# Kernel optimization log

Measured on AMD Instinct MI355X. Metric: run time of the kernel, lower is better.

## Reference

```python
import jax, jax.numpy as jnp
import numpy as np

D = 768
H = 12
HD = 64
S = 77
FF = 3072
EPS = 1e-5


def _layernorm(x, w, b):
    mu = jnp.mean(x, axis=-1, keepdims=True)
    var = jnp.mean(jnp.square(x - mu), axis=-1, keepdims=True)
    return (x - mu) * jax.lax.rsqrt(var + EPS) * w + b


def setup_inputs() -> dict:
    key = jax.random.key(0)
    ks = jax.random.split(key, 18)
    s = 1.0 / np.sqrt(D)
    sf = 1.0 / np.sqrt(FF)
    return {
        "x": jax.random.normal(ks[0], (512, S, D), dtype=jnp.float32),
        "ln1_w": jnp.ones((D,), jnp.float32),
        "ln1_b": jnp.zeros((D,), jnp.float32),
        "qw": jax.random.uniform(ks[1], (D, D), jnp.float32, -s, s),
        "qb": jax.random.uniform(ks[2], (D,), jnp.float32, -s, s),
        "kw": jax.random.uniform(ks[3], (D, D), jnp.float32, -s, s),
        "kb": jax.random.uniform(ks[4], (D,), jnp.float32, -s, s),
        "vw": jax.random.uniform(ks[5], (D, D), jnp.float32, -s, s),
        "vb": jax.random.uniform(ks[6], (D,), jnp.float32, -s, s),
        "ow": jax.random.uniform(ks[7], (D, D), jnp.float32, -s, s),
        "ob": jax.random.uniform(ks[8], (D,), jnp.float32, -s, s),
        "ln2_w": jnp.ones((D,), jnp.float32),
        "ln2_b": jnp.zeros((D,), jnp.float32),
        "fc1_w": jax.random.uniform(ks[9], (FF, D), jnp.float32, -s, s),
        "fc1_b": jax.random.uniform(ks[10], (FF,), jnp.float32, -s, s),
        "fc2_w": jax.random.uniform(ks[11], (D, FF), jnp.float32, -sf, sf),
        "fc2_b": jax.random.uniform(ks[12], (D,), jnp.float32, -sf, sf),
    }


def reference(x, ln1_w, ln1_b, qw, qb, kw, kb, vw, vb, ow, ob,
              ln2_w, ln2_b, fc1_w, fc1_b, fc2_w, fc2_b):
    B = x.shape[0]
    # --- attention block ---
    h = _layernorm(x, ln1_w, ln1_b)
    q = (h @ qw.T + qb) * 0.125
    k = h @ kw.T + kb
    v = h @ vw.T + vb
    # [B, S, H, HD] -> [B, H, S, HD]
    q = q.reshape(B, S, H, HD).transpose(0, 2, 1, 3)
    k = k.reshape(B, S, H, HD).transpose(0, 2, 1, 3)
    v = v.reshape(B, S, H, HD).transpose(0, 2, 1, 3)
    scores = jnp.einsum('bhqd,bhkd->bhqk', q, k)  # [B,H,S,S]
    # causal additive mask: -inf strictly above diagonal
    mask = jnp.triu(jnp.full((S, S), -jnp.inf, dtype=scores.dtype), 1)
    scores = scores + mask
    attn = jax.nn.softmax(scores, axis=-1)
    ctx = jnp.einsum('bhqk,bhkd->bhqd', attn, v)  # [B,H,S,HD]
    ctx = ctx.transpose(0, 2, 1, 3).reshape(B, S, D)
    x = x + (ctx @ ow.T + ob)
    # --- MLP block with QuickGELU ---
    res = x
    h2 = _layernorm(x, ln2_w, ln2_b) @ fc1_w.T + fc1_b
    h2 = h2 * jax.nn.sigmoid(h2 * 1.702)
    return res + (h2 @ fc2_w.T + fc2_b)
```

## Files before the change

### kernel.cpp

```cpp
#include <hip/hip_runtime.h>

typedef unsigned short u16;
typedef __bf16 v8bf __attribute__((ext_vector_type(8)));
typedef unsigned short u16x8 __attribute__((ext_vector_type(8)));
typedef float v4f __attribute__((ext_vector_type(4)));

#define DEV __device__ __forceinline__

constexpr int M_TOK = 512 * 77;

DEV u16 f2bf(float f) {
  union { float f; unsigned int u; } v; v.f = f;
  unsigned int r = v.u + 0x7fffu + ((v.u >> 16) & 1u);
  return (u16)(r >> 16);
}

DEV void gload16(const void* g, void* l) {
  __builtin_amdgcn_global_load_lds((const __attribute__((address_space(1))) void*)g,
                                   (__attribute__((address_space(3))) void*)l, 16, 0, 0);
}

DEV v4f MF(v8bf a, v8bf b, v4f c) {
  return __builtin_amdgcn_mfma_f32_16x16x32_bf16(a, b, c, 0, 0, 0);
}

__global__ void cvt4_k(const float* __restrict__ src, u16* __restrict__ dst, int n4, float scale) {
  int i = blockIdx.x * blockDim.x + threadIdx.x;
  if (i >= n4) return;
  const float4 v = ((const float4*)src)[i];
  ushort4 o;
  o.x = f2bf(v.x * scale); o.y = f2bf(v.y * scale);
  o.z = f2bf(v.z * scale); o.w = f2bf(v.w * scale);
  ((ushort4*)dst)[i] = o;
}

__global__ void qkvb_k(const float* __restrict__ qb, const float* __restrict__ kb,
                       const float* __restrict__ vb, float* __restrict__ dst) {
  int i = blockIdx.x * 256 + threadIdx.x;
  if (i >= 2304) return;
  dst[i] = (i < 768) ? qb[i] * 0.125f : (i < 1536 ? kb[i - 768] : vb[i - 1536]);
}

__global__ __launch_bounds__(256) void ln_k(const float* __restrict__ x, const float* __restrict__ w,
                                            const float* __restrict__ bvec, u16* __restrict__ out, int nrows) {
  const int lane = threadIdx.x & 63;
  const int row = blockIdx.x * 4 + (threadIdx.x >> 6);
  if (row >= nrows) return;
  const float4* xr = (const float4*)(x + (size_t)row * 768);
  float4 v[3];
  float sum = 0.f, sq = 0.f;
#pragma unroll
  for (int t = 0; t < 3; ++t) {
    v[t] = xr[lane + 64 * t];
    sum += v[t].x + v[t].y + v[t].z + v[t].w;
    sq  += v[t].x * v[t].x + v[t].y * v[t].y + v[t].z * v[t].z + v[t].w * v[t].w;
  }
#pragma unroll
  for (int o = 1; o < 64; o <<= 1) { sum += __shfl_xor(sum, o, 64); sq += __shfl_xor(sq, o, 64); }
  const float mean = sum * (1.f / 768.f);
  const float inv = rsqrtf(sq * (1.f / 768.f) - mean * mean + 1e-5f);
  u16* orow = out + (size_t)row * 768;
#pragma unroll
  for (int t = 0; t < 3; ++t) {
    const int c = 4 * (lane + 64 * t);
    ushort4 o4;
    o4.x = f2bf((v[t].x - mean) * inv * w[c + 0] + bvec[c + 0]);
    o4.y = f2bf((v[t].y - mean) * inv * w[c + 1] + bvec[c + 1]);
    o4.z = f2bf((v[t].z - mean) * inv * w[c + 2] + bvec[c + 2]);
    o4.w = f2bf((v[t].w - mean) * inv * w[c + 3] + bvec[c + 3]);
    *(ushort4*)(orow + c) = o4;
  }
}

template <int OUTF32, int ACT, int RES>
__global__ __launch_bounds__(512, 2) void gemm256_k(
    const u16* __restrict__ A, const u16* __restrict__ Bw,
    const float* __restrict__ bias, const float* __restrict__ res,
    void* __restrict__ out, int M, int N, int K, int nbx) {
  __shared__ u16 lds[65536];
  const int tid = threadIdx.x;
  const int lane = tid & 63;
  const int wv = tid >> 6;
  const int wr = wv >> 2, wc = wv & 3;

  const int nwg = gridDim.x;
  const int q = nwg >> 3, r8 = nwg & 7;
  const int xcd = blockIdx.x & 7, cidx = blockIdx.x >> 3;
  const int wg = (xcd < r8 ? xcd * (q + 1) : r8 * (q + 1) + (xcd - r8) * q) + cidx;
  const int m0 = (wg / nbx) * 256;
  const int n0 = (wg % nbx) * 256;

  const int frow = lane & 15;
  const int fq = lane >> 4;
  const int chunkp = (fq ^ (lane & 3) ^ ((lane >> 2) & 3)) & 3;
  const int aRd = (wr * 128 + frow) * 32 + chunkp * 8;
  const int bRd = (wc * 64 + frow) * 32 + chunkp * 8;

  const int srow = tid >> 2;
  const int scg = ((tid & 3) ^ (srow & 3) ^ ((srow >> 2) & 3)) & 3;
  const size_t aBase = (size_t)(m0 + srow) * K + scg * 8;
  const size_t bBase = (size_t)(n0 + srow) * K + scg * 8;
  const int ldsW = wv * 512;

#define GLDA(kt, g) gload16(A + aBase + (size_t)(g) * 128 * K + (kt) * 32, \
                            &lds[(((kt) & 3) << 14) + ((g) << 12) + ldsW])
#define GLDB(kt, g) gload16(Bw + bBase + (size_t)(g) * 128 * K + (kt) * 32, \
                            &lds[(((kt) & 3) << 14) + 8192 + ((g) << 12) + ldsW])
#define BAR() asm volatile("s_barrier" ::: "memory")

  v4f acc[8][4];
#pragma unroll
  for (int i = 0; i < 8; ++i)
#pragma unroll
    for (int j = 0; j < 4; ++j) acc[i][j] = (v4f){0.f, 0.f, 0.f, 0.f};

  const int NT = K >> 5;

  GLDA(0, 0); GLDA(0, 1); GLDB(0, 0); GLDB(0, 1);
  GLDA(1, 0); GLDA(1, 1); GLDB(1, 0); GLDB(1, 1);
  GLDA(2, 0); GLDA(2, 1); GLDB(2, 0); GLDB(2, 1);
  asm volatile("s_waitcnt vmcnt(8)" ::: "memory");
  BAR();

#define KTILE(kt, STG, VM)                                                      \
  do {                                                                          \
    const int sb = ((kt) & 3) << 14;                                            \
    v8bf fa0 = *(const v8bf*)&lds[sb + aRd +    0];                             \
    v8bf fa1 = *(const v8bf*)&lds[sb + aRd +  512];                             \
    v8bf fa2 = *(const v8bf*)&lds[sb + aRd + 1024];                             \
    v8bf fa3 = *(const v8bf*)&lds[sb + aRd + 1536];                             \
    v8bf fb0 = *(const v8bf*)&lds[sb + 8192 + bRd +    0];                      \
    v8bf fb1 = *(const v8bf*)&lds[sb + 8192 + bRd +  512];                      \
    v8bf fb2 = *(const v8bf*)&lds[sb + 8192 + bRd + 1024];                      \
    v8bf fb3 = *(const v8bf*)&lds[sb + 8192 + bRd + 1536];                      \
    if (STG) { GLDA((kt) + 3, 0); GLDA((kt) + 3, 1); }                          \
    BAR();                                                                      \
    __builtin_amdgcn_s_setprio(1);                                              \
    acc[0][0] = MF(fa0, fb0, acc[0][0]); acc[0][1] = MF(fa0, fb1, acc[0][1]);   \
    acc[0][2] = MF(fa0, fb2, acc[0][2]); acc[0][3] = MF(fa0, fb3, acc[0][3]);   \
    acc[1][0] = MF(fa1, fb0, acc[1][0]); acc[1][1] = MF(fa1, fb1, acc[1][1]);   \
    acc[1][2] = MF(fa1, fb2, acc[1][2]); acc[1][3] = MF(fa1, fb3, acc[1][3]);   \
    acc[2][0] = MF(fa2, fb0, acc[2][0]); acc[2][1] = MF(fa2, fb1, acc[2][1]);   \
    acc[2][2] = MF(fa2, fb2, acc[2][2]); acc[2][3] = MF(fa2, fb3, acc[2][3]);   \
    acc[3][0] = MF(fa3, fb0, acc[3][0]); acc[3][1] = MF(fa3, fb1, acc[3][1]);   \
    acc[3][2] = MF(fa3, fb2, acc[3][2]); acc[3][3] = MF(fa3, fb3, acc[3][3]);   \
    __builtin_amdgcn_s_setprio(0);                                              \
    BAR();                                                                      \
    v8bf fa4 = *(const v8bf*)&lds[sb + aRd + 2048];                             \
    v8bf fa5 = *(const v8bf*)&lds[sb + aRd + 2560];                             \
    v8bf fa6 = *(const v8bf*)&lds[sb + aRd + 3072];                             \
    v8bf fa7 = *(const v8bf*)&lds[sb + aRd + 3584];                             \
    if (STG) { GLDB((kt) + 3, 0); GLDB((kt) + 3, 1); }                          \
    if ((VM) == 8) asm volatile("s_waitcnt vmcnt(8)" ::: "memory");             \
    else if ((VM) == 4) asm volatile("s_waitcnt vmcnt(4)" ::: "memory");        \
    else if ((VM) == 0) asm volatile("s_waitcnt vmcnt(0)" ::: "memory");        \
    BAR();                                                                      \
    __builtin_amdgcn_s_setprio(1);                                              \
    acc[4][0] = MF(fa4, fb0, acc[4][0]); acc[4][1] = MF(fa4, fb1, acc[4][1]);   \
    acc[4][2] = MF(fa4, fb2, acc[4][2]); acc[4][3] = MF(fa4, fb3, acc[4][3]);   \
    acc[5][0] = MF(fa5, fb0, acc[5][0]); acc[5][1] = MF(fa5, fb1, acc[5][1]);   \
    acc[5][2] = MF(fa5, fb2, acc[5][2]); acc[5][3] = MF(fa5, fb3, acc[5][3]);   \
    acc[6][0] = MF(fa6, fb0, acc[6][0]); acc[6][1] = MF(fa6, fb1, acc[6][1]);   \
    acc[6][2] = MF(fa6, fb2, acc[6][2]); acc[6][3] = MF(fa6, fb3, acc[6][3]);   \
    acc[7][0] = MF(fa7, fb0, acc[7][0]); acc[7][1] = MF(fa7, fb1, acc[7][1]);   \
    acc[7][2] = MF(fa7, fb2, acc[7][2]); acc[7][3] = MF(fa7, fb3, acc[7][3]);   \
    __builtin_amdgcn_s_setprio(0);                                              \
    BAR();                                                                      \
  } while (0)

  for (int kt = 0; kt + 3 < NT; ++kt) KTILE(kt, 1, 8);
  KTILE(NT - 3, 0, 4);
  KTILE(NT - 2, 0, 0);
  KTILE(NT - 1, 0, -1);
#undef KTILE
#undef GLDA
#undef GLDB
#undef BAR

#pragma unroll
  for (int i = 0; i < 8; ++i) {
    const int rowb = m0 + wr * 128 + i * 16 + fq * 4;
#pragma unroll
    for (int j = 0; j < 4; ++j) {
      const int col = n0 + wc * 64 + j * 16 + frow;
      const float bv = bias[col];
#pragma unroll
      for (int rr = 0; rr < 4; ++rr) {
        float v = acc[i][j][rr] + bv;
        if (ACT) v = v * (1.f / (1.f + __expf(-1.702f * v)));
        const size_t off = (size_t)(rowb + rr) * N + col;
        if (RES) v += res[off];
        if (OUTF32) ((float*)out)[off] = v;
        else ((u16*)out)[off] = f2bf(v);
      }
    }
  }
}

__global__ __launch_bounds__(256) void attn_k(const u16* __restrict__ qkv, u16* __restrict__ ctx) {
  __shared__ u16 sQK[10240];
  __shared__ u16 sVt[64 * 120];
  __shared__ float sS[80][81];
  const int tid = threadIdx.x;
  const int lane = tid & 63;
  const int wv = tid >> 6;
  const int b = blockIdx.x / 12;
  const int h = blockIdx.x % 12;
  u16* sQ = sQK;
  u16* sK = sQK + 5120;
  u16* sP = sQK;

  for (int i = tid; i < 10240 + 64 * 120; i += 256) {
    if (i < 10240) sQK[i] = 0; else sVt[i - 10240] = 0;
  }
  __syncthreads();

  const size_t tokBase = (size_t)(b * 77) * 2304 + h * 64;
  for (int c = tid; c < 77 * 8; c += 256) {
    const int row = c >> 3, k8 = (c & 7) * 8;
    const size_t src = tokBase + (size_t)row * 2304 + k8;
    *(u16x8*)&sQ[row * 64 + k8] = *(const u16x8*)&qkv[src];
    *(u16x8*)&sK[row * 64 + k8] = *(const u16x8*)&qkv[src + 768];
    u16x8 v = *(const u16x8*)&qkv[src + 1536];
#pragma unroll
    for (int j = 0; j < 8; ++j) sVt[(k8 + j) * 120 + row] = v[j];
  }
  __syncthreads();

  const int frow = lane & 15, fk = (lane >> 4) * 8;
  for (int t = wv; t < 25; t += 4) {
    const int it = t / 5, jt = t % 5;
    v4f acc = {0.f, 0.f, 0.f, 0.f};
#pragma unroll
    for (int kk = 0; kk < 2; ++kk) {
      v8bf a = *(const v8bf*)&sQ[(it * 16 + frow) * 64 + kk * 32 + fk];
      v8bf bb = *(const v8bf*)&sK[(jt * 16 + frow) * 64 + kk * 32 + fk];
      acc = MF(a, bb, acc);
    }
    const int col = jt * 16 + frow;
#pragma unroll
    for (int r = 0; r < 4; ++r) {
      const int row = it * 16 + (lane >> 4) * 4 + r;
      sS[row][col] = (col > row) ? -1e30f : acc[r];
    }
  }
  __syncthreads();

  if (tid < 80) {
    const int row = tid;
    float mx = -1e30f;
    for (int c2 = 0; c2 < 80; ++c2) mx = fmaxf(mx, sS[row][c2]);
    float sum = 0.f;
    for (int c2 = 0; c2 < 80; ++c2) { float e = __expf(sS[row][c2] - mx); sum += e; sS[row][c2] = e; }
    const float inv = 1.f / sum;
    for (int c2 = 0; c2 < 80; ++c2) sP[row * 96 + c2] = f2bf(sS[row][c2] * inv);
    for (int c2 = 80; c2 < 96; ++c2) sP[row * 96 + c2] = 0;
  }
  __syncthreads();

  const size_t outBase = (size_t)(b * 77) * 768 + h * 64;
  for (int t = wv; t < 20; t += 4) {
    const int it = t / 4, jt = t % 4;
    v4f acc = {0.f, 0.f, 0.f, 0.f};
#pragma unroll
    for (int kk = 0; kk < 3; ++kk) {
      v8bf a = *(const v8bf*)&sP[(it * 16 + frow) * 96 + kk * 32 + fk];
      v8bf bb = *(const v8bf*)&sVt[(jt * 16 + frow) * 120 + kk * 32 + fk];
      acc = MF(a, bb, acc);
    }
    const int col = jt * 16 + frow;
#pragma unroll
    for (int r = 0; r < 4; ++r) {
      const int row = it * 16 + (lane >> 4) * 4 + r;
      if (row < 77) ctx[outBase + (size_t)row * 768 + col] = f2bf(acc[r]);
    }
  }
}

extern "C" void kernel_launch(void* const* d_in, const int* in_sizes, int n_in,
                              void* d_out, int out_size, void* d_ws, size_t ws_size,
                              hipStream_t stream) {
  const float* x    = (const float*)d_in[0];
  const float* ln1w = (const float*)d_in[1];
  const float* ln1b = (const float*)d_in[2];
  const float* qw   = (const float*)d_in[3];
  const float* qb   = (const float*)d_in[4];
  const float* kw   = (const float*)d_in[5];
  const float* kb   = (const float*)d_in[6];
  const float* vw   = (const float*)d_in[7];
  const float* vb   = (const float*)d_in[8];
  const float* ow   = (const float*)d_in[9];
  const float* ob   = (const float*)d_in[10];
  const float* ln2w = (const float*)d_in[11];
  const float* ln2b = (const float*)d_in[12];
  const float* f1wf = (const float*)d_in[13];
  const float* f1b  = (const float*)d_in[14];
  const float* f2wf = (const float*)d_in[15];
  const float* f2b  = (const float*)d_in[16];
  float* outp = (float*)d_out;

  char* p = (char*)d_ws;
  auto alloc = [&](size_t bytes) { char* r = p; p += (bytes + 255) & ~(size_t)255; return r; };
  u16* wqkv = (u16*)alloc((size_t)2304 * 768 * 2);
  u16* owb  = (u16*)alloc((size_t)768 * 768 * 2);
  u16* f1w  = (u16*)alloc((size_t)3072 * 768 * 2);
  u16* f2w  = (u16*)alloc((size_t)768 * 3072 * 2);
  float* qkvb = (float*)alloc(2304 * 4);
  u16* bufA = (u16*)alloc((size_t)M_TOK * 768 * 2);
  u16* bufB = (u16*)alloc((size_t)M_TOK * 3072 * 2);

  cvt4_k<<<576, 256, 0, stream>>>(qw, wqkv, 147456, 0.125f);
  cvt4_k<<<576, 256, 0, stream>>>(kw, wqkv + 589824, 147456, 1.f);
  cvt4_k<<<576, 256, 0, stream>>>(vw, wqkv + 1179648, 147456, 1.f);
  cvt4_k<<<576, 256, 0, stream>>>(ow, owb, 147456, 1.f);
  cvt4_k<<<2304, 256, 0, stream>>>(f1wf, f1w, 589824, 1.f);
  cvt4_k<<<2304, 256, 0, stream>>>(f2wf, f2w, 589824, 1.f);
  qkvb_k<<<9, 256, 0, stream>>>(qb, kb, vb, qkvb);

  ln_k<<<M_TOK / 4, 256, 0, stream>>>(x, ln1w, ln1b, bufA, M_TOK);
  gemm256_k<0, 0, 0><<<154 * 9, 512, 0, stream>>>(bufA, wqkv, qkvb, nullptr, bufB, M_TOK, 2304, 768, 9);
  attn_k<<<512 * 12, 256, 0, stream>>>(bufB, bufA);
  gemm256_k<1, 0, 1><<<154 * 3, 512, 0, stream>>>(bufA, owb, ob, x, outp, M_TOK, 768, 768, 3);
  ln_k<<<M_TOK / 4, 256, 0, stream>>>(outp, ln2w, ln2b, bufA, M_TOK);
  gemm256_k<0, 1, 0><<<154 * 12, 512, 0, stream>>>(bufA, f1w, f1b, nullptr, bufB, M_TOK, 3072, 768, 12);
  gemm256_k<1, 0, 1><<<154 * 3, 512, 0, stream>>>(bufB, f2w, f2b, outp, outp, M_TOK, 768, 3072, 3);
}
```

Baseline: 976.4 us.

## Shrink GEMM tile to 128x256 with double-buffered LDS and higher occupancy

Reduces the GEMM block tile from 256x256 to 128x256. The LDS pipeline drops from a 4-stage ring to 2-stage double buffering, and launch bounds rise to 4 blocks per CU. The aim is more concurrent blocks and better latency hiding through occupancy, with smaller LDS and register use per block. In exchange, arithmetic intensity per block is lower and prefetch depth is shorter, which may expose global load latency.

```diff
diff --git a/kernel.cpp b/kernel.cpp
--- a/kernel.cpp
+++ b/kernel.cpp
@@ -73,11 +73,11 @@
 }
 
 template <int OUTF32, int ACT, int RES>
-__global__ __launch_bounds__(512, 2) void gemm256_k(
+__global__ __launch_bounds__(512, 4) void gemm_k(
     const u16* __restrict__ A, const u16* __restrict__ Bw,
     const float* __restrict__ bias, const float* __restrict__ res,
     void* __restrict__ out, int M, int N, int K, int nbx) {
-  __shared__ u16 lds[65536];
+  __shared__ u16 lds[24576];
   const int tid = threadIdx.x;
   const int lane = tid & 63;
   const int wv = tid >> 6;
@@ -87,14 +87,14 @@
   const int q = nwg >> 3, r8 = nwg & 7;
   const int xcd = blockIdx.x & 7, cidx = blockIdx.x >> 3;
   const int wg = (xcd < r8 ? xcd * (q + 1) : r8 * (q + 1) + (xcd - r8) * q) + cidx;
-  const int m0 = (wg / nbx) * 256;
+  const int m0 = (wg / nbx) * 128;
   const int n0 = (wg % nbx) * 256;
 
   const int frow = lane & 15;
   const int fq = lane >> 4;
   const int chunkp = (fq ^ (lane & 3) ^ ((lane >> 2) & 3)) & 3;
-  const int aRd = (wr * 128 + frow) * 32 + chunkp * 8;
-  const int bRd = (wc * 64 + frow) * 32 + chunkp * 8;
+  const int aRd = (wr * 64 + frow) * 32 + chunkp * 8;
+  const int bRd = 4096 + (wc * 64 + frow) * 32 + chunkp * 8;
 
   const int srow = tid >> 2;
   const int scg = ((tid & 3) ^ (srow & 3) ^ ((srow >> 2) & 3)) & 3;
@@ -102,39 +102,41 @@
   const size_t bBase = (size_t)(n0 + srow) * K + scg * 8;
   const int ldsW = wv * 512;
 
-#define GLDA(kt, g) gload16(A + aBase + (size_t)(g) * 128 * K + (kt) * 32, \
-                            &lds[(((kt) & 3) << 14) + ((g) << 12) + ldsW])
-#define GLDB(kt, g) gload16(Bw + bBase + (size_t)(g) * 128 * K + (kt) * 32, \
-                            &lds[(((kt) & 3) << 14) + 8192 + ((g) << 12) + ldsW])
+#define GLDA(kt) gload16(A + aBase + (size_t)(kt) * 32, \
+                         &lds[(((kt) & 1) ? 12288 : 0) + ldsW])
+#define GLDB(kt, g) gload16(Bw + bBase + (size_t)(g) * 128 * K + (size_t)(kt) * 32, \
+                            &lds[(((kt) & 1) ? 12288 : 0) + 4096 + ((g) << 12) + ldsW])
 #define BAR() asm volatile("s_barrier" ::: "memory")
 
-  v4f acc[8][4];
-#pragma unroll
-  for (int i = 0; i < 8; ++i)
+  v4f acc[4][4];
+#pragma unroll
+  for (int i = 0; i < 4; ++i)
 #pragma unroll
     for (int j = 0; j < 4; ++j) acc[i][j] = (v4f){0.f, 0.f, 0.f, 0.f};
 
   const int NT = K >> 5;
 
-  GLDA(0, 0); GLDA(0, 1); GLDB(0, 0); GLDB(0, 1);
-  GLDA(1, 0); GLDA(1, 1); GLDB(1, 0); GLDB(1, 1);
-  GLDA(2, 0); GLDA(2, 1); GLDB(2, 0); GLDB(2, 1);
-  asm volatile("s_waitcnt vmcnt(8)" ::: "memory");
+  GLDA(0); GLDB(0, 0); GLDB(0, 1);
+  GLDA(1); GLDB(1, 0); GLDB(1, 1);
+  asm volatile("s_waitcnt vmcnt(3)" ::: "memory");
   BAR();
 
 #define KTILE(kt, STG, VM)                                                      \
   do {                                                                          \
-    const int sb = ((kt) & 3) << 14;                                            \
+    const int sb = ((kt) & 1) ? 12288 : 0;                                      \
     v8bf fa0 = *(const v8bf*)&lds[sb + aRd +    0];                             \
     v8bf fa1 = *(const v8bf*)&lds[sb + aRd +  512];                             \
     v8bf fa2 = *(const v8bf*)&lds[sb + aRd + 1024];                             \
     v8bf fa3 = *(const v8bf*)&lds[sb + aRd + 1536];                             \
-    v8bf fb0 = *(const v8bf*)&lds[sb + 8192 + bRd +    0];                      \
-    v8bf fb1 = *(const v8bf*)&lds[sb + 8192 + bRd +  512];                      \
-    v8bf fb2 = *(const v8bf*)&lds[sb + 8192 + bRd + 1024];                      \
-    v8bf fb3 = *(const v8bf*)&lds[sb + 8192 + bRd + 1536];                      \
-    if (STG) { GLDA((kt) + 3, 0); GLDA((kt) + 3, 1); }                          \
-    BAR();                                                                      \
+    v8bf fb0 = *(const v8bf*)&lds[sb + bRd +    0];                             \
+    v8bf fb1 = *(const v8bf*)&lds[sb + bRd +  512];                             \
+    v8bf fb2 = *(const v8bf*)&lds[sb + bRd + 1024];                             \
+    v8bf fb3 = *(const v8bf*)&lds[sb + bRd + 1536];                             \
+    asm volatile("s_waitcnt lgkmcnt(0)" ::: "memory");                          \
+    BAR();            \
+    if (STG) { GLDA((kt) + 2); GLDB((kt) + 2, 0); GLDB((kt) + 2, 1); }          \
+    if ((VM) == 3) asm volatile("s_waitcnt vmcnt(3)" ::: "memory");             \
+    else if ((VM) == 0) asm volatile("s_waitcnt vmcnt(0)" ::: "memory");        \
     __builtin_amdgcn_s_setprio(1);                                              \
     acc[0][0] = MF(fa0, fb0, acc[0][0]); acc[0][1] = MF(fa0, fb1, acc[0][1]);   \
     acc[0][2] = MF(fa0, fb2, acc[0][2]); acc[0][3] = MF(fa0, fb3, acc[0][3]);   \
@@ -145,31 +147,10 @@
     acc[3][0] = MF(fa3, fb0, acc[3][0]); acc[3][1] = MF(fa3, fb1, acc[3][1]);   \
     acc[3][2] = MF(fa3, fb2, acc[3][2]); acc[3][3] = MF(fa3, fb3, acc[3][3]);   \
     __builtin_amdgcn_s_setprio(0);                                              \
-    BAR();                                                                      \
-    v8bf fa4 = *(const v8bf*)&lds[sb + aRd + 2048];                             \
-    v8bf fa5 = *(const v8bf*)&lds[sb + aRd + 2560];                             \
-    v8bf fa6 = *(const v8bf*)&lds[sb + aRd + 3072];                             \
-    v8bf fa7 = *(const v8bf*)&lds[sb + aRd + 3584];                             \
-    if (STG) { GLDB((kt) + 3, 0); GLDB((kt) + 3, 1); }                          \
-    if ((VM) == 8) asm volatile("s_waitcnt vmcnt(8)" ::: "memory");             \
-    else if ((VM) == 4) asm volatile("s_waitcnt vmcnt(4)" ::: "memory");        \
-    else if ((VM) == 0) asm volatile("s_waitcnt vmcnt(0)" ::: "memory");        \
-    BAR();                                                                      \
-    __builtin_amdgcn_s_setprio(1);                                              \
-    acc[4][0] = MF(fa4, fb0, acc[4][0]); acc[4][1] = MF(fa4, fb1, acc[4][1]);   \
-    acc[4][2] = MF(fa4, fb2, acc[4][2]); acc[4][3] = MF(fa4, fb3, acc[4][3]);   \
-    acc[5][0] = MF(fa5, fb0, acc[5][0]); acc[5][1] = MF(fa5, fb1, acc[5][1]);   \
-    acc[5][2] = MF(fa5, fb2, acc[5][2]); acc[5][3] = MF(fa5, fb3, acc[5][3]);   \
-    acc[6][0] = MF(fa6, fb0, acc[6][0]); acc[6][1] = MF(fa6, fb1, acc[6][1]);   \
-    acc[6][2] = MF(fa6, fb2, acc[6][2]); acc[6][3] = MF(fa6, fb3, acc[6][3]);   \
-    acc[7][0] = MF(fa7, fb0, acc[7][0]); acc[7][1] = MF(fa7, fb1, acc[7][1]);   \
-    acc[7][2] = MF(fa7, fb2, acc[7][2]); acc[7][3] = MF(fa7, fb3, acc[7][3]);   \
-    __builtin_amdgcn_s_setprio(0);                                              \
-    BAR();                                                                      \
+    BAR();              \
   } while (0)
 
-  for (int kt = 0; kt + 3 < NT; ++kt) KTILE(kt, 1, 8);
-  KTILE(NT - 3, 0, 4);
+  for (int kt = 0; kt < NT - 2; ++kt) KTILE(kt, 1, 3);
   KTILE(NT - 2, 0, 0);
   KTILE(NT - 1, 0, -1);
 #undef KTILE
@@ -178,8 +159,8 @@
 #undef BAR
 
 #pragma unroll
-  for (int i = 0; i < 8; ++i) {
-    const int rowb = m0 + wr * 128 + i * 16 + fq * 4;
+  for (int i = 0; i < 4; ++i) {
+    const int rowb = m0 + wr * 64 + i * 16 + fq * 4;
 #pragma unroll
     for (int j = 0; j < 4; ++j) {
       const int col = n0 + wc * 64 + j * 16 + frow;
@@ -318,10 +299,10 @@
   qkvb_k<<<9, 256, 0, stream>>>(qb, kb, vb, qkvb);
 
   ln_k<<<M_TOK / 4, 256, 0, stream>>>(x, ln1w, ln1b, bufA, M_TOK);
-  gemm256_k<0, 0, 0><<<154 * 9, 512, 0, stream>>>(bufA, wqkv, qkvb, nullptr, bufB, M_TOK, 2304, 768, 9);
+  gemm_k<0, 0, 0><<<308 * 9, 512, 0, stream>>>(bufA, wqkv, qkvb, nullptr, bufB, M_TOK, 2304, 768, 9);
   attn_k<<<512 * 12, 256, 0, stream>>>(bufB, bufA);
-  gemm256_k<1, 0, 1><<<154 * 3, 512, 0, stream>>>(bufA, owb, ob, x, outp, M_TOK, 768, 768, 3);
+  gemm_k<1, 0, 1><<<308 * 3, 512, 0, stream>>>(bufA, owb, ob, x, outp, M_TOK, 768, 768, 3);
   ln_k<<<M_TOK / 4, 256, 0, stream>>>(outp, ln2w, ln2b, bufA, M_TOK);
-  gemm256_k<0, 1, 0><<<154 * 12, 512, 0, stream>>>(bufA, f1w, f1b, nullptr, bufB, M_TOK, 3072, 768, 12);
-  gemm256_k<1, 0, 1><<<154 * 3, 512, 0, stream>>>(bufB, f2w, f2b, outp, outp, M_TOK, 768, 3072, 3);
-}
+  gemm_k<0, 1, 0><<<308 * 12, 512, 0, stream>>>(bufA, f1w, f1b, nullptr, bufB, M_TOK, 3072, 768, 12);
+  gemm_k<1, 0, 1><<<308 * 3, 512, 0, stream>>>(bufB, f2w, f2b, outp, outp, M_TOK, 768, 3072, 3);
+}
```

Result: no change. 967.5 us (-0.9%).

## Restructure 256x256 GEMM main loop to 64-wide K tiles with double buffering

Applied to the files above, without the earlier changes.

The GEMM main loop now stages 64-element K tiles in two LDS buffers instead of four 32-wide stages. It uses 128-byte rows with an 8-way XOR swizzle, and interleaves the global-to-LDS loads for the next tile with the MFMA quarters of the current one. The aim is fewer barriers and waitcnts per unit of K, wider and better-coalesced loads, and fewer LDS bank conflicts. In exchange, less data is in flight (two buffers instead of three tiles ahead), and K must be a multiple of 128.

```diff
diff --git a/kernel.cpp b/kernel.cpp
--- a/kernel.cpp
+++ b/kernel.cpp
@@ -84,29 +84,36 @@
   const int wr = wv >> 2, wc = wv & 3;
 
   const int nwg = gridDim.x;
-  const int q = nwg >> 3, r8 = nwg & 7;
+  const int q8 = nwg >> 3, r8 = nwg & 7;
   const int xcd = blockIdx.x & 7, cidx = blockIdx.x >> 3;
-  const int wg = (xcd < r8 ? xcd * (q + 1) : r8 * (q + 1) + (xcd - r8) * q) + cidx;
+  const int wg = (xcd < r8 ? xcd * (q8 + 1) : r8 * (q8 + 1) + (xcd - r8) * q8) + cidx;
   const int m0 = (wg / nbx) * 256;
   const int n0 = (wg % nbx) * 256;
 
-  const int frow = lane & 15;
-  const int fq = lane >> 4;
-  const int chunkp = (fq ^ (lane & 3) ^ ((lane >> 2) & 3)) & 3;
-  const int aRd = (wr * 128 + frow) * 32 + chunkp * 8;
-  const int bRd = (wc * 64 + frow) * 32 + chunkp * 8;
-
-  const int srow = tid >> 2;
-  const int scg = ((tid & 3) ^ (srow & 3) ^ ((srow >> 2) & 3)) & 3;
-  const size_t aBase = (size_t)(m0 + srow) * K + scg * 8;
-  const size_t bBase = (size_t)(n0 + srow) * K + scg * 8;
+  const int frow = lane & 15, fq = lane >> 4;
+  const int e = frow & 7;
+  const int aB0 = wr * 8192 + frow * 64 + ((fq ^ e) * 8);
+  const int aB1 = aB0 ^ 32;
+  const int bB0 = 16384 + wc * 4096 + frow * 64 + ((fq ^ e) * 8);
+  const int bB1 = bB0 ^ 32;
+
+  const int srow = tid >> 3;
+  const int cOff = ((tid & 7) ^ (srow & 7)) * 8;
+  const u16* pA = A + (size_t)(m0 + srow) * K + cOff;
+  const u16* pB = Bw + (size_t)(n0 + srow) * K + cOff;
+  const size_t qk = (size_t)K * 64;
   const int ldsW = wv * 512;
 
-#define GLDA(kt, g) gload16(A + aBase + (size_t)(g) * 128 * K + (kt) * 32, \
-                            &lds[(((kt) & 3) << 14) + ((g) << 12) + ldsW])
-#define GLDB(kt, g) gload16(Bw + bBase + (size_t)(g) * 128 * K + (kt) * 32, \
-                            &lds[(((kt) & 3) << 14) + 8192 + ((g) << 12) + ldsW])
+#define LD(IDX) (*(const v8bf*)&lds[IDX])
 #define BAR() asm volatile("s_barrier" ::: "memory")
+#define VM2() asm volatile("s_waitcnt vmcnt(2)" ::: "memory")
+#define VM0() asm volatile("s_waitcnt vmcnt(0)" ::: "memory")
+#define P1() __builtin_amdgcn_s_setprio(1)
+#define P0() __builtin_amdgcn_s_setprio(0)
+#define MM4(ii) acc[ii][0] = MF(fa##ii, fb0, acc[ii][0]); \
+                acc[ii][1] = MF(fa##ii, fb1, acc[ii][1]); \
+                acc[ii][2] = MF(fa##ii, fb2, acc[ii][2]); \
+                acc[ii][3] = MF(fa##ii, fb3, acc[ii][3])
 
   v4f acc[8][4];
 #pragma unroll
@@ -114,68 +121,90 @@
 #pragma unroll
     for (int j = 0; j < 4; ++j) acc[i][j] = (v4f){0.f, 0.f, 0.f, 0.f};
 
-  const int NT = K >> 5;
-
-  GLDA(0, 0); GLDA(0, 1); GLDB(0, 0); GLDB(0, 1);
-  GLDA(1, 0); GLDA(1, 1); GLDB(1, 0); GLDB(1, 1);
-  GLDA(2, 0); GLDA(2, 1); GLDB(2, 0); GLDB(2, 1);
-  asm volatile("s_waitcnt vmcnt(8)" ::: "memory");
-  BAR();
-
-#define KTILE(kt, STG, VM)                                                      \
-  do {                                                                          \
-    const int sb = ((kt) & 3) << 14;                                            \
-    v8bf fa0 = *(const v8bf*)&lds[sb + aRd +    0];                             \
-    v8bf fa1 = *(const v8bf*)&lds[sb + aRd +  512];                             \
-    v8bf fa2 = *(const v8bf*)&lds[sb + aRd + 1024];                             \
-    v8bf fa3 = *(const v8bf*)&lds[sb + aRd + 1536];                             \
-    v8bf fb0 = *(const v8bf*)&lds[sb + 8192 + bRd +    0];                      \
-    v8bf fb1 = *(const v8bf*)&lds[sb + 8192 + bRd +  512];                      \
-    v8bf fb2 = *(const v8bf*)&lds[sb + 8192 + bRd + 1024];                      \
-    v8bf fb3 = *(const v8bf*)&lds[sb + 8192 + bRd + 1536];                      \
-    if (STG) { GLDA((kt) + 3, 0); GLDA((kt) + 3, 1); }                          \
-    BAR();                                                                      \
-    __builtin_amdgcn_s_setprio(1);                                              \
-    acc[0][0] = MF(fa0, fb0, acc[0][0]); acc[0][1] = MF(fa0, fb1, acc[0][1]);   \
-    acc[0][2] = MF(fa0, fb2, acc[0][2]); acc[0][3] = MF(fa0, fb3, acc[0][3]);   \
-    acc[1][0] = MF(fa1, fb0, acc[1][0]); acc[1][1] = MF(fa1, fb1, acc[1][1]);   \
-    acc[1][2] = MF(fa1, fb2, acc[1][2]); acc[1][3] = MF(fa1, fb3, acc[1][3]);   \
-    acc[2][0] = MF(fa2, fb0, acc[2][0]); acc[2][1] = MF(fa2, fb1, acc[2][1]);   \
-    acc[2][2] = MF(fa2, fb2, acc[2][2]); acc[2][3] = MF(fa2, fb3, acc[2][3]);   \
-    acc[3][0] = MF(fa3, fb0, acc[3][0]); acc[3][1] = MF(fa3, fb1, acc[3][1]);   \
-    acc[3][2] = MF(fa3, fb2, acc[3][2]); acc[3][3] = MF(fa3, fb3, acc[3][3]);   \
-    __builtin_amdgcn_s_setprio(0);                                              \
-    BAR();                                                                      \
-    v8bf fa4 = *(const v8bf*)&lds[sb + aRd + 2048];                             \
-    v8bf fa5 = *(const v8bf*)&lds[sb + aRd + 2560];                             \
-    v8bf fa6 = *(const v8bf*)&lds[sb + aRd + 3072];                             \
-    v8bf fa7 = *(const v8bf*)&lds[sb + aRd + 3584];                             \
-    if (STG) { GLDB((kt) + 3, 0); GLDB((kt) + 3, 1); }                          \
-    if ((VM) == 8) asm volatile("s_waitcnt vmcnt(8)" ::: "memory");             \
-    else if ((VM) == 4) asm volatile("s_waitcnt vmcnt(4)" ::: "memory");        \
-    else if ((VM) == 0) asm volatile("s_waitcnt vmcnt(0)" ::: "memory");        \
-    BAR();                                                                      \
-    __builtin_amdgcn_s_setprio(1);                                              \
-    acc[4][0] = MF(fa4, fb0, acc[4][0]); acc[4][1] = MF(fa4, fb1, acc[4][1]);   \
-    acc[4][2] = MF(fa4, fb2, acc[4][2]); acc[4][3] = MF(fa4, fb3, acc[4][3]);   \
-    acc[5][0] = MF(fa5, fb0, acc[5][0]); acc[5][1] = MF(fa5, fb1, acc[5][1]);   \
-    acc[5][2] = MF(fa5, fb2, acc[5][2]); acc[5][3] = MF(fa5, fb3, acc[5][3]);   \
-    acc[6][0] = MF(fa6, fb0, acc[6][0]); acc[6][1] = MF(fa6, fb1, acc[6][1]);   \
-    acc[6][2] = MF(fa6, fb2, acc[6][2]); acc[6][3] = MF(fa6, fb3, acc[6][3]);   \
-    acc[7][0] = MF(fa7, fb0, acc[7][0]); acc[7][1] = MF(fa7, fb1, acc[7][1]);   \
-    acc[7][2] = MF(fa7, fb2, acc[7][2]); acc[7][3] = MF(fa7, fb3, acc[7][3]);   \
-    __builtin_amdgcn_s_setprio(0);                                              \
-    BAR();                                                                      \
-  } while (0)
-
-  for (int kt = 0; kt + 3 < NT; ++kt) KTILE(kt, 1, 8);
-  KTILE(NT - 3, 0, 4);
-  KTILE(NT - 2, 0, 0);
-  KTILE(NT - 1, 0, -1);
-#undef KTILE
-#undef GLDA
-#undef GLDB
+  const int NT = K >> 6;
+
+  gload16(pA + 0 * qk, &lds[0 + ldsW]);
+  gload16(pA + 2 * qk, &lds[8192 + ldsW]);
+  gload16(pB + 0 * qk, &lds[16384 + ldsW]);
+  gload16(pB + 1 * qk, &lds[20480 + ldsW]);
+  gload16(pB + 2 * qk, &lds[24576 + ldsW]);
+  gload16(pB + 3 * qk, &lds[28672 + ldsW]);
+  gload16(pA + 1 * qk, &lds[4096 + ldsW]);
+  gload16(pA + 3 * qk, &lds[12288 + ldsW]);
+  VM2(); BAR();
+
+  for (int kt = 0; kt < NT; kt += 2) {
+    const u16* PA1 = pA + (size_t)(kt + 1) * 64;
+    const u16* PB1 = pB + (size_t)(kt + 1) * 64;
+    const u16* PA2 = PA1 + 64;
+    const u16* PB2 = PB1 + 64;
+    const int STG2 = (kt + 2 < NT);
+    v8bf fa0, fa1, fa2, fa3, fa4, fa5, fa6, fa7, fb0, fb1, fb2, fb3;
+
+    fb0 = LD(bB0); fb1 = LD(bB0 + 1024); fb2 = LD(bB0 + 2048); fb3 = LD(bB0 + 3072);
+    fa0 = LD(aB0); fa1 = LD(aB0 + 1024); fa2 = LD(aB0 + 2048); fa3 = LD(aB0 + 3072);
+    gload16(PA1 + 0 * qk, &lds[32768 + 0 + ldsW]);
+    gload16(PA1 + 2 * qk, &lds[32768 + 8192 + ldsW]);
+    VM2(); BAR();
+    P1(); MM4(0); MM4(1); MM4(2); MM4(3); P0(); BAR();
+    fa4 = LD(aB0 + 4096); fa5 = LD(aB0 + 5120); fa6 = LD(aB0 + 6144); fa7 = LD(aB0 + 7168);
+    gload16(PB1 + 0 * qk, &lds[32768 + 16384 + ldsW]);
+    gload16(PB1 + 1 * qk, &lds[32768 + 20480 + ldsW]);
+    BAR();
+    P1(); MM4(4); MM4(5); MM4(6); MM4(7); P0(); BAR();
+    fb0 = LD(bB1); fb1 = LD(bB1 + 1024); fb2 = LD(bB1 + 2048); fb3 = LD(bB1 + 3072);
+    fa0 = LD(aB1); fa1 = LD(aB1 + 1024); fa2 = LD(aB1 + 2048); fa3 = LD(aB1 + 3072);
+    gload16(PB1 + 2 * qk, &lds[32768 + 24576 + ldsW]);
+    gload16(PB1 + 3 * qk, &lds[32768 + 28672 + ldsW]);
+    BAR();
+    P1(); MM4(0); MM4(1); MM4(2); MM4(3); P0(); BAR();
+    fa4 = LD(aB1 + 4096); fa5 = LD(aB1 + 5120); fa6 = LD(aB1 + 6144); fa7 = LD(aB1 + 7168);
+    gload16(PA1 + 1 * qk, &lds[32768 + 4096 + ldsW]);
+    gload16(PA1 + 3 * qk, &lds[32768 + 12288 + ldsW]);
+    VM2(); BAR();
+    P1(); MM4(4); MM4(5); MM4(6); MM4(7); P0(); BAR();
+    fb0 = LD(32768 + bB0); fb1 = LD(32768 + bB0 + 1024); fb2 = LD(32768 + bB0 + 2048); fb3 = LD(32768 + bB0 + 3072);
+    fa0 = LD(32768 + aB0); fa1 = LD(32768 + aB0 + 1024); fa2 = LD(32768 + aB0 + 2048); fa3 = LD(32768 + aB0 + 3072);
+    if (STG2) {
+      gload16(PA2 + 0 * qk, &lds[0 + ldsW]);
+      gload16(PA2 + 2 * qk, &lds[8192 + ldsW]);
+      VM2();
+    } else {
+      VM0();
+    }
+    BAR();
+    P1(); MM4(0); MM4(1); MM4(2); MM4(3); P0(); BAR();
+    fa4 = LD(32768 + aB0 + 4096); fa5 = LD(32768 + aB0 + 5120); fa6 = LD(32768 + aB0 + 6144); fa7 = LD(32768 + aB0 + 7168);
+    if (STG2) {
+      gload16(PB2 + 0 * qk, &lds[16384 + ldsW]);
+      gload16(PB2 + 1 * qk, &lds[20480 + ldsW]);
+    }
+    BAR();
+    P1(); MM4(4); MM4(5); MM4(6); MM4(7); P0(); BAR();
+    fb0 = LD(32768 + bB1); fb1 = LD(32768 + bB1 + 1024); fb2 = LD(32768 + bB1 + 2048); fb3 = LD(32768 + bB1 + 3072);
+    fa0 = LD(32768 + aB1); fa1 = LD(32768 + aB1 + 1024); fa2 = LD(32768 + aB1 + 2048); fa3 = LD(32768 + aB1 + 3072);
+    if (STG2) {
+      gload16(PB2 + 2 * qk, &lds[24576 + ldsW]);
+      gload16(PB2 + 3 * qk, &lds[28672 + ldsW]);
+    }
+    BAR();
+    P1(); MM4(0); MM4(1); MM4(2); MM4(3); P0(); BAR();
+    fa4 = LD(32768 + aB1 + 4096); fa5 = LD(32768 + aB1 + 5120); fa6 = LD(32768 + aB1 + 6144); fa7 = LD(32768 + aB1 + 7168);
+    if (STG2) {
+      gload16(PA2 + 1 * qk, &lds[4096 + ldsW]);
+      gload16(PA2 + 3 * qk, &lds[12288 + ldsW]);
+      VM2();
+    }
+    BAR();
+    P1(); MM4(4); MM4(5); MM4(6); MM4(7); P0(); BAR();
+  }
+#undef LD
 #undef BAR
+#undef VM2
+#undef VM0
+#undef P1
+#undef P0
+#undef MM4
 
 #pragma unroll
   for (int i = 0; i < 8; ++i) {
```

New measurement: 955.1 us. -2.2%, faster.
